# Kernel tuning notes

Hardware: AMD Instinct MI355X
Metric: run time of the kernel (lower is better)

The kernel has to match this reference:

```python
import jax, jax.numpy as jnp
import numpy as np
from jax import lax

EPS = 1e-5

def conv2d(x, w):
    # x: [B,C,H,W], w: [O,I,kh,kw], VALID, stride 1
    return lax.conv_general_dilated(x, w, (1, 1), 'VALID',
                                    dimension_numbers=('NCHW', 'OIHW', 'NCHW'))

def bn_eval(x, g, b, m, v):
    # per-channel eval-mode batchnorm on NCHW
    scale = g / jnp.sqrt(v + EPS)
    return x * scale[None, :, None, None] + (b - m * scale)[None, :, None, None]

def xcorr_depthwise(search, kernel):
    # search: [B,C,Hs,Ws], kernel: [B,C,hk,wk] -> [B,C,Ho,Wo]
    B, C, Hs, Ws = search.shape
    hk, wk = kernel.shape[2], kernel.shape[3]
    s = search.reshape(1, B * C, Hs, Ws)
    k = kernel.reshape(B * C, 1, hk, wk)
    out = lax.conv_general_dilated(s, k, (1, 1), 'VALID',
                                   dimension_numbers=('NCHW', 'OIHW', 'NCHW'),
                                   feature_group_count=B * C)
    return out.reshape(B, C, out.shape[2], out.shape[3])

def setup_inputs() -> dict:
    key = jax.random.key(0)
    ks = jax.random.split(key, 16)
    B, C, HID, OUT = 64, 256, 256, 10
    d = {}
    d['kernel'] = jax.random.normal(ks[0], (B, C, 7, 7), jnp.float32)
    d['search'] = jax.random.normal(ks[1], (B, C, 31, 31), jnp.float32)
    # conv_kernel branch
    d['ck_w'] = jax.random.normal(ks[2], (HID, C, 3, 3), jnp.float32) * 0.02
    d['ck_g'] = jnp.ones((HID,), jnp.float32)
    d['ck_b'] = jnp.zeros((HID,), jnp.float32)
    d['ck_m'] = jax.random.normal(ks[3], (HID,), jnp.float32) * 0.1
    d['ck_v'] = jax.random.uniform(ks[4], (HID,), jnp.float32, 0.5, 1.5)
    # conv_search branch
    d['cs_w'] = jax.random.normal(ks[5], (HID, C, 3, 3), jnp.float32) * 0.02
    d['cs_g'] = jnp.ones((HID,), jnp.float32)
    d['cs_b'] = jnp.zeros((HID,), jnp.float32)
    d['cs_m'] = jax.random.normal(ks[6], (HID,), jnp.float32) * 0.1
    d['cs_v'] = jax.random.uniform(ks[7], (HID,), jnp.float32, 0.5, 1.5)
    # head: 1x1 conv (no bias) + BN + ReLU + 1x1 conv (bias)
    d['h1_w'] = jax.random.normal(ks[8], (HID, HID), jnp.float32) * 0.05
    d['h_g'] = jnp.ones((HID,), jnp.float32)
    d['h_b'] = jnp.zeros((HID,), jnp.float32)
    d['h_m'] = jax.random.normal(ks[9], (HID,), jnp.float32) * 0.1
    d['h_v'] = jax.random.uniform(ks[10], (HID,), jnp.float32, 0.5, 1.5)
    d['h2_w'] = jax.random.normal(ks[11], (OUT, HID), jnp.float32) * 0.05
    d['h2_b'] = jnp.zeros((OUT,), jnp.float32)
    return d

def reference(kernel, search, ck_w, ck_g, ck_b, ck_m, ck_v,
              cs_w, cs_g, cs_b, cs_m, cs_v,
              h1_w, h_g, h_b, h_m, h_v, h2_w, h2_b):
    k = jax.nn.relu(bn_eval(conv2d(kernel, ck_w), ck_g, ck_b, ck_m, ck_v))   # [B,256,5,5]
    s = jax.nn.relu(bn_eval(conv2d(search, cs_w), cs_g, cs_b, cs_m, cs_v))   # [B,256,29,29]
    feat = xcorr_depthwise(s, k)                                             # [B,256,25,25]
    x = jnp.einsum('oi,bihw->bohw', h1_w, feat)
    x = jax.nn.relu(bn_eval(x, h_g, h_b, h_m, h_v))
    out = jnp.einsum('oi,bihw->bohw', h2_w, x) + h2_b[None, :, None, None]   # [B,10,25,25]
    return out
```

## Files before the change

### kernel.cpp

```cpp
#include <hip/hip_runtime.h>
#include <cstddef>
#include <cstdint>

#define BN_EPS 1e-5f

typedef __attribute__((ext_vector_type(8))) __bf16 bf16x8;
typedef __attribute__((ext_vector_type(4))) float f32x4;

__device__ inline unsigned short f2bf(float f) {
    unsigned u = __builtin_bit_cast(unsigned, f);
    unsigned r = (u + 0x7fff + ((u >> 16) & 1)) >> 16;
    return (unsigned short)r;
}

#define GLDS16(g, l)                                                        \
    __builtin_amdgcn_global_load_lds(                                       \
        (const __attribute__((address_space(1))) void*)(g),                 \
        (__attribute__((address_space(3))) void*)(l), 16, 0, 0)

template<int H, int W>
__device__ inline void nhwc_body(int bh, const float* __restrict__ in,
                                 unsigned short* __restrict__ out)
{
    const int b = bh / H, h = bh - b * H;
    const int c = threadIdx.x;
    const float* src = in + ((size_t)(b * 256 + c) * H + h) * W;
    unsigned short* dst = out + (size_t)bh * W * 256 + c;
    #pragma unroll
    for (int w = 0; w < W; ++w) dst[w * 256] = f2bf(src[w]);
}

__global__ __launch_bounds__(256)
void prep_kernel(const float* __restrict__ srch, const float* __restrict__ kin,
                 const float* __restrict__ cs_w, const float* __restrict__ ck_w,
                 const float* __restrict__ h1_w, const float* __restrict__ h2_w,
                 unsigned short* __restrict__ s16, unsigned short* __restrict__ k16,
                 unsigned short* __restrict__ wTs, unsigned short* __restrict__ wTk,
                 unsigned short* __restrict__ h1w16, unsigned short* __restrict__ h2w16,
                 int G31, int G7)
{
    const int bid = blockIdx.x;
    if (bid < G31) {
        nhwc_body<31, 31>(bid, srch, s16);
    } else if (bid < G31 + G7) {
        nhwc_body<7, 7>(bid - G31, kin, k16);
    } else {
        const int i = (bid - G31 - G7) * 256 + threadIdx.x;
        if (i < 589824) {
            const int ic = i & 255, t = i >> 8, oc = t & 255, khkw = t >> 8;
            wTs[i] = f2bf(cs_w[(size_t)((oc << 8) + ic) * 9 + khkw]);
        } else if (i < 1179648) {
            const int j = i - 589824;
            const int ic = j & 255, t = j >> 8, oc = t & 255, khkw = t >> 8;
            wTk[j] = f2bf(ck_w[(size_t)((oc << 8) + ic) * 9 + khkw]);
        } else if (i < 1245184) {
            const int j = i - 1179648;
            h1w16[j] = f2bf(h1_w[j]);
        } else if (i < 1249280) {
            const int j = i - 1245184;
            const int oc = j >> 8, ic = j & 255;
            h2w16[j] = (oc < 10) ? f2bf(h2_w[oc * 256 + ic]) : (unsigned short)0;
        }
    }
}

struct ConvParams {
    const unsigned short* bsrc;
    const unsigned short* wT;
    const float *bg, *bb, *bm, *bv;
    float* out;
    int IH, IW, OW, PPB, N;
};

__global__ __launch_bounds__(256)
void conv3x3_kernel(ConvParams S, ConvParams K, int Gs)
{
    __shared__ __align__(16) unsigned short Alds[128 * 64];
    __shared__ __align__(16) unsigned short Blds[128 * 64];

    const int tid  = threadIdx.x;
    const int lane = tid & 63;
    const int wid  = tid >> 6;

    const int raw = blockIdx.x;
    ConvParams P;
    int tileid;
    if (raw < Gs) {
        P = S;
        const int q = Gs >> 3, r = Gs & 7;
        const int xcd = raw & 7, seq = raw >> 3;
        tileid = (xcd < r ? xcd * (q + 1) : r * (q + 1) + (xcd - r) * q) + seq;
    } else {
        P = K;
        tileid = raw - Gs;
    }
    const int pt  = tileid >> 1;
    const int oct = tileid & 1;
    const int oc0 = oct << 7;
    const int p0  = pt << 7;

    int aoff[4], brow[4], bgs8[4], ldsrow[4];
    #pragma unroll
    for (int i = 0; i < 4; ++i) {
        const int r  = i * 32 + wid * 8 + (lane >> 3);
        const int gs = (lane & 7) ^ (r & 7);
        aoff[i] = (oc0 + r) * 256 + gs * 8;
        int pg = p0 + r; if (pg > P.N - 1) pg = P.N - 1;
        const int bb_ = pg / P.PPB;
        const int p   = pg - bb_ * P.PPB;
        const int oh  = p / P.OW, ow = p - oh * P.OW;
        brow[i] = (bb_ * P.IH + oh) * P.IW + ow;
        bgs8[i] = gs * 8;
        ldsrow[i] = (i * 32 + wid * 8) * 64;
    }

    const int q_  = lane >> 4;
    const int lr  = lane & 15;
    const int wm0 = (wid >> 1) * 64;
    const int wn0 = (wid & 1) * 64;
    const int g0  = q_ ^ (lane & 7);
    const int g1  = (4 + q_) ^ (lane & 7);
    const unsigned short* Abase = &Alds[(wm0 + lr) * 64];
    const unsigned short* Bbase = &Blds[(wn0 + lr) * 64];

    f32x4 acc[4][4] = {};

    int kh = 0, kw = 0;
    for (int khkw = 0; khkw < 9; ++khkw) {
        const size_t wslice = (size_t)khkw << 16;
        const int tapadd = kh * P.IW + kw;
        for (int ics = 0; ics < 4; ++ics) {
            const int ic0 = ics * 64;
            __syncthreads();
            #pragma unroll
            for (int i = 0; i < 4; ++i) {
                GLDS16(P.wT + wslice + aoff[i] + ic0, &Alds[ldsrow[i]]);
                GLDS16(P.bsrc + (size_t)(brow[i] + tapadd) * 256 + ic0 + bgs8[i],
                       &Blds[ldsrow[i]]);
            }
            __syncthreads();

            bf16x8 bfr[4][2];
            #pragma unroll
            for (int n = 0; n < 4; ++n) {
                bfr[n][0] = *(const bf16x8*)(Bbase + n * 1024 + g0 * 8);
                bfr[n][1] = *(const bf16x8*)(Bbase + n * 1024 + g1 * 8);
            }
            #pragma unroll
            for (int m = 0; m < 4; ++m) {
                bf16x8 a0 = *(const bf16x8*)(Abase + m * 1024 + g0 * 8);
                bf16x8 a1 = *(const bf16x8*)(Abase + m * 1024 + g1 * 8);
                #pragma unroll
                for (int n = 0; n < 4; ++n) {
                    acc[m][n] = __builtin_amdgcn_mfma_f32_16x16x32_bf16(
                                    a0, bfr[n][0], acc[m][n], 0, 0, 0);
                    acc[m][n] = __builtin_amdgcn_mfma_f32_16x16x32_bf16(
                                    a1, bfr[n][1], acc[m][n], 0, 0, 0);
                }
            }
        }
        if (++kw == 3) { kw = 0; ++kh; }
    }

    #pragma unroll
    for (int m = 0; m < 4; ++m) {
        const int ocm = oc0 + wm0 + m * 16 + q_ * 4;
        float sc[4], sh[4];
        #pragma unroll
        for (int r = 0; r < 4; ++r) {
            sc[r] = P.bg[ocm + r] * rsqrtf(P.bv[ocm + r] + BN_EPS);
            sh[r] = P.bb[ocm + r] - P.bm[ocm + r] * sc[r];
        }
        #pragma unroll
        for (int n = 0; n < 4; ++n) {
            const int pg = p0 + wn0 + n * 16 + lr;
            if (pg < P.N) {
                const int bb_ = pg / P.PPB;
                const int p   = pg - bb_ * P.PPB;
                #pragma unroll
                for (int r = 0; r < 4; ++r)
                    P.out[((size_t)(bb_ * 256 + ocm + r)) * P.PPB + p] =
                        fmaxf(acc[m][n][r] * sc[r] + sh[r], 0.f);
            }
        }
    }
}

template<int KH, int KW, int IH, int IW, int OW, int PPB, bool OUT_NT>
__global__ __launch_bounds__(256)
void conv_mfma_kernel(const unsigned short* __restrict__ bsrc,
                      const unsigned short* __restrict__ wT,
                      const float* __restrict__ bn_g,
                      const float* __restrict__ bn_b,
                      const float* __restrict__ bn_m,
                      const float* __restrict__ bn_v,
                      float* __restrict__ out_f32,
                      unsigned short* __restrict__ out_nt,
                      int N)
{
    constexpr int KHW = KH * KW;
    __shared__ __align__(16) unsigned short Alds[128 * 64];
    __shared__ __align__(16) unsigned short Blds[128 * 64];

    const int tid  = threadIdx.x;
    const int lane = tid & 63;
    const int wid  = tid >> 6;

    const int NPT = (N + 127) >> 7;
    const int bid = blockIdx.x;
    const int pt  = bid % NPT;
    const int oct = bid / NPT;
    const int oc0 = oct * 128;
    const int p0  = pt * 128;

    int aoff[4], brow[4], bgs8[4], ldsrow[4];
    #pragma unroll
    for (int i = 0; i < 4; ++i) {
        const int r  = i * 32 + wid * 8 + (lane >> 3);
        const int gs = (lane & 7) ^ (r & 7);
        aoff[i] = (oc0 + r) * 256 + gs * 8;
        int pg = p0 + r; if (pg > N - 1) pg = N - 1;
        const int bb = pg / PPB;
        const int p  = pg - bb * PPB;
        const int oh = p / OW, ow = p - oh * OW;
        brow[i] = (bb * IH + oh) * IW + ow;
        bgs8[i] = gs * 8;
        ldsrow[i] = (i * 32 + wid * 8) * 64;
    }

    const int q   = lane >> 4;
    const int lr  = lane & 15;
    const int wm0 = (wid >> 1) * 64;
    const int wn0 = (wid & 1) * 64;
    const int g0  = q ^ (lane & 7);
    const int g1  = (4 + q) ^ (lane & 7);
    const unsigned short* Abase = &Alds[(wm0 + lr) * 64];
    const unsigned short* Bbase = &Blds[(wn0 + lr) * 64];

    f32x4 acc[4][4] = {};

    for (int khkw = 0; khkw < KHW; ++khkw) {
        const int kh = khkw / KW;
        const int kw = khkw - kh * KW;
        const size_t wslice = (size_t)khkw * 65536;
        const int tapadd = kh * IW + kw;
        for (int ics = 0; ics < 4; ++ics) {
            const int ic0 = ics * 64;
            __syncthreads();
            #pragma unroll
            for (int i = 0; i < 4; ++i) {
                GLDS16(wT + wslice + aoff[i] + ic0, &Alds[ldsrow[i]]);
                GLDS16(bsrc + (size_t)(brow[i] + tapadd) * 256 + ic0 + bgs8[i],
                       &Blds[ldsrow[i]]);
            }
            __syncthreads();

            bf16x8 bfr[4][2];
            #pragma unroll
            for (int n = 0; n < 4; ++n) {
                bfr[n][0] = *(const bf16x8*)(Bbase + n * 1024 + g0 * 8);
                bfr[n][1] = *(const bf16x8*)(Bbase + n * 1024 + g1 * 8);
            }
            #pragma unroll
            for (int m = 0; m < 4; ++m) {
                bf16x8 a0 = *(const bf16x8*)(Abase + m * 1024 + g0 * 8);
                bf16x8 a1 = *(const bf16x8*)(Abase + m * 1024 + g1 * 8);
                #pragma unroll
                for (int n = 0; n < 4; ++n) {
                    acc[m][n] = __builtin_amdgcn_mfma_f32_16x16x32_bf16(
                                    a0, bfr[n][0], acc[m][n], 0, 0, 0);
                    acc[m][n] = __builtin_amdgcn_mfma_f32_16x16x32_bf16(
                                    a1, bfr[n][1], acc[m][n], 0, 0, 0);
                }
            }
        }
    }

    #pragma unroll
    for (int m = 0; m < 4; ++m) {
        const int ocm = oc0 + wm0 + m * 16 + q * 4;
        float sc[4], sh[4];
        #pragma unroll
        for (int r = 0; r < 4; ++r) {
            sc[r] = bn_g[ocm + r] * rsqrtf(bn_v[ocm + r] + BN_EPS);
            sh[r] = bn_b[ocm + r] - bn_m[ocm + r] * sc[r];
        }
        #pragma unroll
        for (int n = 0; n < 4; ++n) {
            const int pg = p0 + wn0 + n * 16 + lr;
            if (pg < N) {
                if (OUT_NT) {
                    unsigned e0 = f2bf(fmaxf(acc[m][n][0] * sc[0] + sh[0], 0.f));
                    unsigned e1 = f2bf(fmaxf(acc[m][n][1] * sc[1] + sh[1], 0.f));
                    unsigned e2 = f2bf(fmaxf(acc[m][n][2] * sc[2] + sh[2], 0.f));
                    unsigned e3 = f2bf(fmaxf(acc[m][n][3] * sc[3] + sh[3], 0.f));
                    uint2 v; v.x = e0 | (e1 << 16); v.y = e2 | (e3 << 16);
                    *(uint2*)(out_nt + (size_t)pg * 256 + ocm) = v;
                } else {
                    const int bb = pg / PPB;
                    const int p  = pg - bb * PPB;
                    #pragma unroll
                    for (int r = 0; r < 4; ++r)
                        out_f32[((size_t)(bb * 256 + ocm + r)) * PPB + p] =
                            fmaxf(acc[m][n][r] * sc[r] + sh[r], 0.f);
                }
            }
        }
    }
}

__global__ __launch_bounds__(256)
void xcorr_kernel(const float* __restrict__ sf, const float* __restrict__ kf,
                  unsigned short* __restrict__ xc2)
{
    const int bid = blockIdx.x;
    const int b = bid >> 5, cg = bid & 31;
    const int c0 = cg * 8;
    __shared__ float ss[8][841];
    __shared__ float kk[8][25];
    const int tid = threadIdx.x;
    {
        const int cl = tid >> 5, ln = tid & 31;
        const float* sp = sf + ((size_t)(b * 256 + c0 + cl)) * 841;
        for (int j = ln; j < 841; j += 32) ss[cl][j] = sp[j];
        if (tid < 200) {
            const int c = tid / 25, j = tid - c * 25;
            kk[c][j] = kf[((size_t)(b * 256 + c0 + c)) * 25 + j];
        }
    }
    __syncthreads();
    const int cc = tid & 7, tp = tid >> 3;
    for (int p = tp; p < 625; p += 32) {
        const int oh = p / 25, ow = p - oh * 25;
        const float* s = &ss[cc][oh * 29 + ow];
        float acc = 0.f;
        #pragma unroll
        for (int i = 0; i < 5; ++i)
            #pragma unroll
            for (int j = 0; j < 5; ++j)
                acc += s[i * 29 + j] * kk[cc][i * 5 + j];
        xc2[((size_t)(b * 625 + p)) * 256 + c0 + cc] = f2bf(acc);
    }
}

__global__ __launch_bounds__(256)
void head2_mfma_kernel(const unsigned short* __restrict__ y,
                       const unsigned short* __restrict__ h2w16,
                       const float* __restrict__ h2b,
                       float* __restrict__ out, int N)
{
    const int tid = threadIdx.x, lane = tid & 63, wid = tid >> 6;
    const int pbase = blockIdx.x * 256 + wid * 64;
    const int q = lane >> 4, lr = lane & 15;

    const unsigned short* arow = h2w16 + lr * 256 + q * 8;
    const unsigned short* yrow[4];
    #pragma unroll
    for (int n = 0; n < 4; ++n) {
        int pg = pbase + n * 16 + lr; if (pg > N - 1) pg = N - 1;
        yrow[n] = y + (size_t)pg * 256 + q * 8;
    }

    f32x4 acc[4] = {};
    #pragma unroll
    for (int ks = 0; ks < 8; ++ks) {
        bf16x8 a = *(const bf16x8*)(arow + ks * 32);
        #pragma unroll
        for (int n = 0; n < 4; ++n) {
            bf16x8 bb = *(const bf16x8*)(yrow[n] + ks * 32);
            acc[n] = __builtin_amdgcn_mfma_f32_16x16x32_bf16(a, bb, acc[n], 0, 0, 0);
        }
    }

    #pragma unroll
    for (int n = 0; n < 4; ++n) {
        const int pg = pbase + n * 16 + lr;
        if (pg < N) {
            const int b = pg / 625, p = pg - b * 625;
            #pragma unroll
            for (int r = 0; r < 4; ++r) {
                const int oc = q * 4 + r;
                if (oc < 10)
                    out[((size_t)(b * 10 + oc)) * 625 + p] = acc[n][r] + h2b[oc];
            }
        }
    }
}

extern "C" void kernel_launch(void* const* d_in, const int* in_sizes, int n_in,
                              void* d_out, int out_size, void* d_ws, size_t ws_size,
                              hipStream_t stream)
{
    const float* kin  = (const float*)d_in[0];
    const float* srch = (const float*)d_in[1];
    const float* ck_w = (const float*)d_in[2];
    const float* ck_g = (const float*)d_in[3];
    const float* ck_b = (const float*)d_in[4];
    const float* ck_m = (const float*)d_in[5];
    const float* ck_v = (const float*)d_in[6];
    const float* cs_w = (const float*)d_in[7];
    const float* cs_g = (const float*)d_in[8];
    const float* cs_b = (const float*)d_in[9];
    const float* cs_m = (const float*)d_in[10];
    const float* cs_v = (const float*)d_in[11];
    const float* h1_w = (const float*)d_in[12];
    const float* h_g  = (const float*)d_in[13];
    const float* h_b  = (const float*)d_in[14];
    const float* h_m  = (const float*)d_in[15];
    const float* h_v  = (const float*)d_in[16];
    const float* h2_w = (const float*)d_in[17];
    const float* h2_b = (const float*)d_in[18];

    const int B = in_sizes[0] / (256 * 7 * 7);

    uint8_t* w = (uint8_t*)d_ws;
    unsigned short* s16   = (unsigned short*)(w);
    unsigned short* xc2   = (unsigned short*)(w);
    float*          sf    = (float*)(w + 31490048);
    unsigned short* y     = (unsigned short*)(w + 31490048);
    float*          kf    = (float*)(w + 86605824);
    unsigned short* k16   = (unsigned short*)(w + 88244224);
    unsigned short* wTk   = (unsigned short*)(w + 89849856);
    unsigned short* wTs   = (unsigned short*)(w + 91029504);
    unsigned short* h1w16 = (unsigned short*)(w + 92209152);
    unsigned short* h2w16 = (unsigned short*)(w + 92340224);

    const int Ns = B * 841;
    const int Nk = B * 25;
    const int Nh = B * 625;
    const int Gs = 2 * ((Ns + 127) / 128);
    const int Gk = 2 * ((Nk + 127) / 128);
    const int G31 = B * 31, G7 = B * 7;

    dim3 blk(256, 1, 1);

    hipLaunchKernelGGL(prep_kernel, dim3(G31 + G7 + 4880), blk, 0, stream,
                       srch, kin, cs_w, ck_w, h1_w, h2_w,
                       s16, k16, wTs, wTk, h1w16, h2w16, G31, G7);

    ConvParams S{ s16, wTs, cs_g, cs_b, cs_m, cs_v, sf, 31, 31, 29, 841, Ns };
    ConvParams K{ k16, wTk, ck_g, ck_b, ck_m, ck_v, kf, 7, 7, 5, 25, Nk };
    hipLaunchKernelGGL(conv3x3_kernel, dim3(Gs + Gk), blk, 0, stream, S, K, Gs);

    hipLaunchKernelGGL(xcorr_kernel, dim3(B * 32), blk, 0, stream, sf, kf, xc2);

    hipLaunchKernelGGL((conv_mfma_kernel<1, 1, 25, 25, 25, 625, true>),
                       dim3(2 * ((Nh + 127) / 128)), blk, 0, stream,
                       xc2, h1w16, h_g, h_b, h_m, h_v, (float*)nullptr, y, Nh);

    hipLaunchKernelGGL(head2_mfma_kernel, dim3((Nh + 255) / 256), blk, 0, stream,
                       y, h2w16, h2_b, (float*)d_out, Nh);
}
```

Measured before the change: 176.4 us.

## Store conv features as NHWC bf16 and rewrite xcorr with register accumulation

The 3x3 conv epilogue now writes bf16 features in NHWC order using packed 8-byte stores, replacing the fp32 NCHW output. The depthwise cross-correlation is rewritten so that each thread owns one channel and one output row, reads bf16 NHWC data with coalesced loads, and accumulates 25 outputs in registers without LDS staging. The NHWC transpose in the prep kernel now goes through an LDS tile so that global reads are coalesced. These changes aim to cut the memory traffic of the feature tensors and the strided uncoalesced accesses, at the cost of extra bf16 rounding of intermediate features and higher register pressure in the xcorr kernel.

```diff
diff --git a/kernel.cpp b/kernel.cpp
--- a/kernel.cpp
+++ b/kernel.cpp
@@ -12,22 +12,35 @@
     unsigned r = (u + 0x7fff + ((u >> 16) & 1)) >> 16;
     return (unsigned short)r;
 }
+__device__ inline float bf2f(unsigned short u) {
+    return __builtin_bit_cast(float, (unsigned)u << 16);
+}
 
 #define GLDS16(g, l)                                                        \
     __builtin_amdgcn_global_load_lds(                                       \
         (const __attribute__((address_space(1))) void*)(g),                 \
         (__attribute__((address_space(3))) void*)(l), 16, 0, 0)
 
-template<int H, int W>
+template<int H, int W, int WP>
 __device__ inline void nhwc_body(int bh, const float* __restrict__ in,
                                  unsigned short* __restrict__ out)
 {
+    __shared__ unsigned short tl[256][WP];
+    const int tid = threadIdx.x;
     const int b = bh / H, h = bh - b * H;
-    const int c = threadIdx.x;
-    const float* src = in + ((size_t)(b * 256 + c) * H + h) * W;
-    unsigned short* dst = out + (size_t)bh * W * 256 + c;
-    #pragma unroll
-    for (int w = 0; w < W; ++w) dst[w * 256] = f2bf(src[w]);
+    const int g = tid >> 5, wl = tid & 31;
+    const float* base = in + (size_t)b * 256 * (H * W) + (size_t)h * W;
+    if (wl < W) {
+        #pragma unroll
+        for (int cc = 0; cc < 32; ++cc) {
+            const int c = cc * 8 + g;
+            tl[c][wl] = f2bf(base[(size_t)c * (H * W) + wl]);
+        }
+    }
+    __syncthreads();
+    unsigned short* dst = out + (size_t)bh * W * 256 + tid;
+    #pragma unroll
+    for (int w = 0; w < W; ++w) dst[w * 256] = tl[tid][w];
 }
 
 __global__ __launch_bounds__(256)
@@ -41,9 +54,9 @@
 {
     const int bid = blockIdx.x;
     if (bid < G31) {
-        nhwc_body<31, 31>(bid, srch, s16);
+        nhwc_body<31, 31, 33>(bid, srch, s16);
     } else if (bid < G31 + G7) {
-        nhwc_body<7, 7>(bid - G31, kin, k16);
+        nhwc_body<7, 7, 9>(bid - G31, kin, k16);
     } else {
         const int i = (bid - G31 - G7) * 256 + threadIdx.x;
         if (i < 589824) {
@@ -68,7 +81,7 @@
     const unsigned short* bsrc;
     const unsigned short* wT;
     const float *bg, *bb, *bm, *bv;
-    float* out;
+    unsigned short* out;
     int IH, IW, OW, PPB, N;
 };
 
@@ -87,9 +100,9 @@
     int tileid;
     if (raw < Gs) {
         P = S;
-        const int q = Gs >> 3, r = Gs & 7;
+        const int q8 = Gs >> 3, r8 = Gs & 7;
         const int xcd = raw & 7, seq = raw >> 3;
-        tileid = (xcd < r ? xcd * (q + 1) : r * (q + 1) + (xcd - r) * q) + seq;
+        tileid = (xcd < r8 ? xcd * (q8 + 1) : r8 * (q8 + 1) + (xcd - r8) * q8) + seq;
     } else {
         P = K;
         tileid = raw - Gs;
@@ -175,15 +188,52 @@
         for (int n = 0; n < 4; ++n) {
             const int pg = p0 + wn0 + n * 16 + lr;
             if (pg < P.N) {
-                const int bb_ = pg / P.PPB;
-                const int p   = pg - bb_ * P.PPB;
-                #pragma unroll
-                for (int r = 0; r < 4; ++r)
-                    P.out[((size_t)(bb_ * 256 + ocm + r)) * P.PPB + p] =
-                        fmaxf(acc[m][n][r] * sc[r] + sh[r], 0.f);
-            }
-        }
-    }
+                unsigned e0 = f2bf(fmaxf(acc[m][n][0] * sc[0] + sh[0], 0.f));
+                unsigned e1 = f2bf(fmaxf(acc[m][n][1] * sc[1] + sh[1], 0.f));
+                unsigned e2 = f2bf(fmaxf(acc[m][n][2] * sc[2] + sh[2], 0.f));
+                unsigned e3 = f2bf(fmaxf(acc[m][n][3] * sc[3] + sh[3], 0.f));
+                uint2 v; v.x = e0 | (e1 << 16); v.y = e2 | (e3 << 16);
+                *(uint2*)(P.out + (size_t)pg * 256 + ocm) = v;
+            }
+        }
+    }
+}
+
+__global__ __launch_bounds__(256)
+void xcorr_nhwc_kernel(const unsigned short* __restrict__ sfeat,
+                       const unsigned short* __restrict__ kfeat,
+                       unsigned short* __restrict__ xc2)
+{
+    const int bid = blockIdx.x;
+    const int b = bid / 25, oh = bid - b * 25;
+    const int c = threadIdx.x;
+
+    float kv[25];
+    const unsigned short* kp = kfeat + (size_t)b * 25 * 256 + c;
+    #pragma unroll
+    for (int t = 0; t < 25; ++t) kv[t] = bf2f(kp[t * 256]);
+
+    float acc[25];
+    #pragma unroll
+    for (int ow = 0; ow < 25; ++ow) acc[ow] = 0.f;
+
+    const unsigned short* sp = sfeat + ((size_t)(b * 29 + oh)) * 29 * 256 + c;
+    #pragma unroll
+    for (int i = 0; i < 5; ++i) {
+        #pragma unroll
+        for (int w = 0; w < 29; ++w) {
+            const float sv = bf2f(sp[(i * 29 + w) * 256]);
+            #pragma unroll
+            for (int j = 0; j < 5; ++j) {
+                if (j <= w && w - j <= 24)
+                    acc[w - j] += sv * kv[i * 5 + j];
+            }
+        }
+    }
+
+    unsigned short* op = xc2 + ((size_t)(b * 625 + oh * 25)) * 256 + c;
+    #pragma unroll
+    for (int ow = 0; ow < 25; ++ow) op[ow * 256] = f2bf(acc[ow]);
 }
 
 template<int KH, int KW, int IH, int IW, int OW, int PPB, bool OUT_NT>
@@ -217,14 +267,14 @@
     #pragma unroll
     for (int i = 0; i < 4; ++i) {
         const int r  = i * 32 + wid * 8 + (lane >> 3);
-        const int gs = (lane & 7) ^ (r & 7);
-        aoff[i] = (oc0 + r) * 256 + gs * 8;
+        const int gsv = (lane & 7) ^ (r & 7);
+        aoff[i] = (oc0 + r) * 256 + gsv * 8;
         int pg = p0 + r; if (pg > N - 1) pg = N - 1;
         const int bb = pg / PPB;
         const int p  = pg - bb * PPB;
         const int oh = p / OW, ow = p - oh * OW;
         brow[i] = (bb * IH + oh) * IW + ow;
-        bgs8[i] = gs * 8;
+        bgs8[i] = gsv * 8;
         ldsrow[i] = (i * 32 + wid * 8) * 64;
     }
 
@@ -306,40 +356,6 @@
                 }
             }
         }
-    }
-}
-
-__global__ __launch_bounds__(256)
-void xcorr_kernel(const float* __restrict__ sf, const float* __restrict__ kf,
-                  unsigned short* __restrict__ xc2)
-{
-    const int bid = blockIdx.x;
-    const int b = bid >> 5, cg = bid & 31;
-    const int c0 = cg * 8;
-    __shared__ float ss[8][841];
-    __shared__ float kk[8][25];
-    const int tid = threadIdx.x;
-    {
-        const int cl = tid >> 5, ln = tid & 31;
-        const float* sp = sf + ((size_t)(b * 256 + c0 + cl)) * 841;
-        for (int j = ln; j < 841; j += 32) ss[cl][j] = sp[j];
-        if (tid < 200) {
-            const int c = tid / 25, j = tid - c * 25;
-            kk[c][j] = kf[((size_t)(b * 256 + c0 + c)) * 25 + j];
-        }
-    }
-    __syncthreads();
-    const int cc = tid & 7, tp = tid >> 3;
-    for (int p = tp; p < 625; p += 32) {
-        const int oh = p / 25, ow = p - oh * 25;
-        const float* s = &ss[cc][oh * 29 + ow];
-        float acc = 0.f;
-        #pragma unroll
-        for (int i = 0; i < 5; ++i)
-            #pragma unroll
-            for (int j = 0; j < 5; ++j)
-                acc += s[i * 29 + j] * kk[cc][i * 5 + j];
-        xc2[((size_t)(b * 625 + p)) * 256 + c0 + cc] = f2bf(acc);
     }
 }
 
@@ -414,16 +430,16 @@
     const int B = in_sizes[0] / (256 * 7 * 7);
 
     uint8_t* w = (uint8_t*)d_ws;
-    unsigned short* s16   = (unsigned short*)(w);
-    unsigned short* xc2   = (unsigned short*)(w);
-    float*          sf    = (float*)(w + 31490048);
-    unsigned short* y     = (unsigned short*)(w + 31490048);
-    float*          kf    = (float*)(w + 86605824);
-    unsigned short* k16   = (unsigned short*)(w + 88244224);
-    unsigned short* wTk   = (unsigned short*)(w + 89849856);
-    unsigned short* wTs   = (unsigned short*)(w + 91029504);
-    unsigned short* h1w16 = (unsigned short*)(w + 92209152);
-    unsigned short* h2w16 = (unsigned short*)(w + 92340224);
+    unsigned short* s16     = (unsigned short*)(w);
+    unsigned short* xc2     = (unsigned short*)(w);
+    unsigned short* sfeat16 = (unsigned short*)(w + 31490048);
+    unsigned short* y       = (unsigned short*)(w + 31490048);
+    unsigned short* kf16    = (unsigned short*)(w + 59047936);
+    unsigned short* k16     = (unsigned short*)(w + 59867136);
+    unsigned short* wTk     = (unsigned short*)(w + 61472768);
+    unsigned short* wTs     = (unsigned short*)(w + 62652416);
+    unsigned short* h1w16   = (unsigned short*)(w + 63832064);
+    unsigned short* h2w16   = (unsigned short*)(w + 63963136);
 
     const int Ns = B * 841;
     const int Nk = B * 25;
@@ -438,11 +454,12 @@
                        srch, kin, cs_w, ck_w, h1_w, h2_w,
                        s16, k16, wTs, wTk, h1w16, h2w16, G31, G7);
 
-    ConvParams S{ s16, wTs, cs_g, cs_b, cs_m, cs_v, sf, 31, 31, 29, 841, Ns };
-    ConvParams K{ k16, wTk, ck_g, ck_b, ck_m, ck_v, kf, 7, 7, 5, 25, Nk };
+    ConvParams S{ s16, wTs, cs_g, cs_b, cs_m, cs_v, sfeat16, 31, 31, 29, 841, Ns };
+    ConvParams K{ k16, wTk, ck_g, ck_b, ck_m, ck_v, kf16, 7, 7, 5, 25, Nk };
     hipLaunchKernelGGL(conv3x3_kernel, dim3(Gs + Gk), blk, 0, stream, S, K, Gs);
 
-    hipLaunchKernelGGL(xcorr_kernel, dim3(B * 32), blk, 0, stream, sf, kf, xc2);
+    hipLaunchKernelGGL(xcorr_nhwc_kernel, dim3(B * 25), blk, 0, stream,
+                       sfeat16, kf16, xc2);
 
     hipLaunchKernelGGL((conv_mfma_kernel<1, 1, 25, 25, 25, 625, true>),
                        dim3(2 * ((Nh + 127) / 128)), blk, 0, stream,
```

Measured after the change: 176.6 us. Within noise of the previous version (+0.1%).
